# Optimization experiments

Hardware: AMD Instinct MI355X
Metric: run time of the kernel (lower is better)

The kernel has to match this reference:

```python
import jax, jax.numpy as jnp
import numpy as np

B, H, S, D = 4, 16, 2048, 128

def setup_inputs() -> dict:
    key = jax.random.key(0)
    kq, kk, kv = jax.random.split(key, 3)
    q = jax.random.normal(kq, (B, H, S, D), dtype=jnp.float32)
    k = jax.random.normal(kk, (B, H, S, D), dtype=jnp.float32)
    v = jax.random.normal(kv, (B, H, S, D), dtype=jnp.float32)
    return {"q": q, "k": k, "v": v}

def reference(q, k, v):
    # scores: [B, H, S, S] -- NOTE: original module applies no 1/sqrt(D) scale
    scores = jnp.einsum("bhqd,bhkd->bhqk", q, k)
    a = jax.nn.softmax(scores, axis=-1)  # numerically stable softmax
    return jnp.einsum("bhqk,bhkd->bhqd", a, v)
```

## Files before the change

kernel.cpp:

```cpp
#include <hip/hip_runtime.h>
#include <hip/hip_bf16.h>


#define QBLK   64
#define KVBLK  64
#define DHEAD  128
#define SEQ    2048
#define KPAD   136
#define PPAD   72

typedef _Float16 f16x8 __attribute__((ext_vector_type(8)));
typedef _Float16 f16x4 __attribute__((ext_vector_type(4)));
typedef float    f32x4 __attribute__((ext_vector_type(4)));

#define AS1P(x) ((const __attribute__((address_space(1))) void*)(size_t)(x))
#define AS3P(x) ((__attribute__((address_space(3))) void*)(unsigned long long)(unsigned)(size_t)(x))

__global__ __launch_bounds__(256)
void preconv_kernel(const float* __restrict__ K, const float* __restrict__ V,
                    _Float16* __restrict__ Kp, _Float16* __restrict__ Vp) {
    const int bt = blockIdx.x;
    const size_t src = (size_t)bt * (KVBLK * DHEAD);
    const float* Kt = K + src;
    const float* Vt = V + src;
    _Float16* Ko = Kp + src;
    _Float16* Vo = Vp + src;
    #pragma unroll
    for (int j = 0; j < 4; ++j) {
        const int c = threadIdx.x + 256 * j;
        {
            const int row = c >> 4;
            const int d0  = (c & 15) * 8;
            float4 f0 = *(const float4*)(Kt + row * DHEAD + d0);
            float4 f1 = *(const float4*)(Kt + row * DHEAD + d0 + 4);
            f16x8 h;
            h[0]=(_Float16)f0.x; h[1]=(_Float16)f0.y; h[2]=(_Float16)f0.z; h[3]=(_Float16)f0.w;
            h[4]=(_Float16)f1.x; h[5]=(_Float16)f1.y; h[6]=(_Float16)f1.z; h[7]=(_Float16)f1.w;
            *(f16x8*)&Ko[row * 128 + (d0 ^ ((row & 7) << 3))] = h;
        }
        {
            const int d8  = (c & 1) | (((c >> 3) & 7) << 1);
            const int row = ((c >> 1) & 3) | ((c >> 6) << 2);
            const int d0  = d8 * 8;
            float4 f0 = *(const float4*)(Vt + row * DHEAD + d0);
            float4 f1 = *(const float4*)(Vt + row * DHEAD + d0 + 4);
            f16x8 h;
            h[0]=(_Float16)f0.x; h[1]=(_Float16)f0.y; h[2]=(_Float16)f0.z; h[3]=(_Float16)f0.w;
            h[4]=(_Float16)f1.x; h[5]=(_Float16)f1.y; h[6]=(_Float16)f1.z; h[7]=(_Float16)f1.w;
            const int st = (row >> 2) * 8 + (d0 >> 4);
            *(f16x8*)&Vo[st * 64 + (row & 3) * 16 + (d0 & 15)] = h;
        }
    }
}

__global__ __launch_bounds__(256, 3)
void attn_fwd_kernel(const float* __restrict__ Q, const _Float16* __restrict__ Kp,
                     const _Float16* __restrict__ Vp, float* __restrict__ O) {
    __shared__ __align__(16) _Float16 K_lds[KVBLK * DHEAD];
    __shared__ __align__(16) _Float16 V_lds[KVBLK * DHEAD];
    __shared__ __align__(16) _Float16 P_lds[4 * 16 * 64];

    const int tid  = threadIdx.x;
    const int lane = tid & 63;
    const int wave = tid >> 6;
    const int g    = lane >> 4;
    const int lg   = lane & 15;

    const int flat    = blockIdx.x + gridDim.x * blockIdx.y;
    const int newflat = (flat & 7) * 256 + (flat >> 3);
    const int qtile   = newflat & 31;
    const int bh      = newflat >> 5;

    const float* Qg = Q + (size_t)bh * SEQ * DHEAD + (size_t)(qtile * QBLK) * DHEAD;
    float*       Og = O + (size_t)bh * SEQ * DHEAD + (size_t)(qtile * QBLK) * DHEAD;

    const unsigned trbase = (unsigned)(size_t)&V_lds[0] + (unsigned)(g * 2048 + lg * 8);

    f16x8 qf[4];
    {
        const float* qrow = Qg + (size_t)(wave * 16 + lg) * DHEAD;
        #pragma unroll
        for (int dc = 0; dc < 4; ++dc) {
            const int d0 = dc * 32 + g * 8;
            float4 f0 = *(const float4*)(qrow + d0);
            float4 f1 = *(const float4*)(qrow + d0 + 4);
            qf[dc][0] = (_Float16)f0.x; qf[dc][1] = (_Float16)f0.y;
            qf[dc][2] = (_Float16)f0.z; qf[dc][3] = (_Float16)f0.w;
            qf[dc][4] = (_Float16)f1.x; qf[dc][5] = (_Float16)f1.y;
            qf[dc][6] = (_Float16)f1.z; qf[dc][7] = (_Float16)f1.w;
        }
    }

    f32x4 acc[8];
    #pragma unroll
    for (int dt = 0; dt < 8; ++dt) { acc[dt][0]=0.f; acc[dt][1]=0.f; acc[dt][2]=0.f; acc[dt][3]=0.f; }
    float m = -1e30f, l = 0.f;

    for (int t = 0; t < SEQ / KVBLK; ++t) {
        {
            const _Float16* Ktile = Kp + (size_t)(bh * 32 + t) * (KVBLK * DHEAD);
            const _Float16* Vtile = Vp + (size_t)(bh * 32 + t) * (KVBLK * DHEAD);
            #pragma unroll
            for (int i = 0; i < 4; ++i) {
                const int eoff = wave * 2048 + i * 512;
                __builtin_amdgcn_global_load_lds(AS1P(Ktile + eoff + lane * 8),
                                                 AS3P(&K_lds[eoff]), 16, 0, 0);
                __builtin_amdgcn_global_load_lds(AS1P(Vtile + eoff + lane * 8),
                                                 AS3P(&V_lds[eoff]), 16, 0, 0);
            }
        }
        __syncthreads();

        f32x4 s[4];
        __builtin_amdgcn_s_setprio(1);
        #pragma unroll
        for (int ct = 0; ct < 4; ++ct) {
            f32x4 a; a[0]=0.f; a[1]=0.f; a[2]=0.f; a[3]=0.f;
            #pragma unroll
            for (int dc = 0; dc < 4; ++dc) {
                const int krow = ct * 16 + lg;
                const int off  = krow * 128 + ((dc * 32 + g * 8) ^ ((krow & 7) << 3));
                f16x8 kh = *(const f16x8*)&K_lds[off];
                a = __builtin_amdgcn_mfma_f32_16x16x32_f16(kh, qf[dc], a, 0, 0, 0);
            }
            s[ct] = a;
        }
        __builtin_amdgcn_s_setprio(0);

        float pmax = s[0][0];
        #pragma unroll
        for (int ct = 0; ct < 4; ++ct)
            #pragma unroll
            for (int r = 0; r < 4; ++r)
                pmax = fmaxf(pmax, s[ct][r]);
        pmax = fmaxf(pmax, __shfl_xor(pmax, 16));
        pmax = fmaxf(pmax, __shfl_xor(pmax, 32));
        const float mnew = fmaxf(m, pmax);
        const float sc   = __expf(m - mnew);
        m = mnew;
        float rs = 0.f;
        #pragma unroll
        for (int ct = 0; ct < 4; ++ct)
            #pragma unroll
            for (int r = 0; r < 4; ++r) {
                float p = __expf(s[ct][r] - mnew);
                s[ct][r] = p;
                rs += p;
            }
        rs += __shfl_xor(rs, 16);
        rs += __shfl_xor(rs, 32);
        l = l * sc + rs;

        #pragma unroll
        for (int r = 0; r < 4; ++r) {
            const float scr = __shfl(sc, g * 20 + r);
            #pragma unroll
            for (int dt = 0; dt < 8; ++dt) acc[dt][r] *= scr;
        }

        _Float16* pbase = &P_lds[wave * 16 * 64];
        #pragma unroll
        for (int ct = 0; ct < 4; ++ct) {
            f16x4 pk;
            pk[0] = (_Float16)s[ct][0]; pk[1] = (_Float16)s[ct][1];
            pk[2] = (_Float16)s[ct][2]; pk[3] = (_Float16)s[ct][3];
            *(f16x4*)&pbase[lg * 64 + ((ct * 16 + g * 4) ^ ((lg & 7) << 3))] = pk;
        }

        #pragma unroll
        for (int kt = 0; kt < 2; ++kt) {
            f16x8 pf = *(const f16x8*)&pbase[lg * 64 + ((kt * 32 + g * 8) ^ ((lg & 7) << 3))];
            #pragma unroll
            for (int dp = 0; dp < 4; ++dp) {
                f16x4 a0, a1, b0, b1;
                asm volatile(
                    "ds_read_b64_tr_b16 %0, %4 offset:%5\n\t"
                    "ds_read_b64_tr_b16 %1, %4 offset:%6\n\t"
                    "ds_read_b64_tr_b16 %2, %4 offset:%7\n\t"
                    "ds_read_b64_tr_b16 %3, %4 offset:%8\n\t"
                    "s_waitcnt lgkmcnt(0)"
                    : "=&v"(a0), "=&v"(a1), "=&v"(b0), "=&v"(b1)
                    : "v"(trbase),
                      "i"(kt * 8192 + (dp * 2 + 0) * 128),
                      "i"(kt * 8192 + 1024 + (dp * 2 + 0) * 128),
                      "i"(kt * 8192 + (dp * 2 + 1) * 128),
                      "i"(kt * 8192 + 1024 + (dp * 2 + 1) * 128)
                    : "memory");
                __builtin_amdgcn_sched_barrier(0);
                f16x8 vf0 = __builtin_shufflevector(a0, a1, 0, 1, 2, 3, 4, 5, 6, 7);
                f16x8 vf1 = __builtin_shufflevector(b0, b1, 0, 1, 2, 3, 4, 5, 6, 7);
                __builtin_amdgcn_s_setprio(1);
                acc[dp * 2 + 0] = __builtin_amdgcn_mfma_f32_16x16x32_f16(pf, vf0, acc[dp * 2 + 0], 0, 0, 0);
                acc[dp * 2 + 1] = __builtin_amdgcn_mfma_f32_16x16x32_f16(pf, vf1, acc[dp * 2 + 1], 0, 0, 0);
                __builtin_amdgcn_s_setprio(0);
            }
        }
        __syncthreads();
    }

    const float linv = 1.f / l;
    float inv[4];
    #pragma unroll
    for (int r = 0; r < 4; ++r) inv[r] = __shfl(linv, g * 20 + r);
    float* ob = Og + (size_t)(wave * 16) * DHEAD;
    #pragma unroll
    for (int dt = 0; dt < 8; ++dt)
        #pragma unroll
        for (int r = 0; r < 4; ++r)
            ob[(size_t)(g * 4 + r) * DHEAD + dt * 16 + lg] = acc[dt][r] * inv[r];
}

__global__ __launch_bounds__(256, 3)
void attn_fwd_legacy(const float* __restrict__ Q, const float* __restrict__ K,
                     const float* __restrict__ V, float* __restrict__ O) {
    __shared__ __align__(16) _Float16 K_lds[KVBLK * KPAD];
    __shared__ __align__(16) _Float16 V_lds[KVBLK * DHEAD];
    __shared__ __align__(16) _Float16 P_lds[4 * 16 * PPAD];

    const int tid  = threadIdx.x;
    const int lane = tid & 63;
    const int wave = tid >> 6;
    const int g    = lane >> 4;
    const int lg   = lane & 15;

    const int flat    = blockIdx.x + gridDim.x * blockIdx.y;
    const int newflat = (flat & 7) * 256 + (flat >> 3);
    const int qtile   = newflat & 31;
    const int bh      = newflat >> 5;

    const size_t base = (size_t)bh * SEQ * DHEAD;
    const float* Qg = Q + base + (size_t)(qtile * QBLK) * DHEAD;
    const float* Kg = K + base;
    const float* Vg = V + base;
    float*       Og = O + base + (size_t)(qtile * QBLK) * DHEAD;

    const unsigned trbase = (unsigned)(size_t)&V_lds[0] + (unsigned)(g * 2048 + lg * 8);

    f16x8 qf[4];
    {
        const float* qrow = Qg + (size_t)(wave * 16 + lg) * DHEAD;
        #pragma unroll
        for (int dc = 0; dc < 4; ++dc) {
            const int d0 = dc * 32 + g * 8;
            float4 f0 = *(const float4*)(qrow + d0);
            float4 f1 = *(const float4*)(qrow + d0 + 4);
            qf[dc][0] = (_Float16)f0.x; qf[dc][1] = (_Float16)f0.y;
            qf[dc][2] = (_Float16)f0.z; qf[dc][3] = (_Float16)f0.w;
            qf[dc][4] = (_Float16)f1.x; qf[dc][5] = (_Float16)f1.y;
            qf[dc][6] = (_Float16)f1.z; qf[dc][7] = (_Float16)f1.w;
        }
    }

    f32x4 acc[8];
    #pragma unroll
    for (int dt = 0; dt < 8; ++dt) { acc[dt][0]=0.f; acc[dt][1]=0.f; acc[dt][2]=0.f; acc[dt][3]=0.f; }
    float m = -1e30f, l = 0.f;

    for (int t = 0; t < SEQ / KVBLK; ++t) {
        {
            const float* Kt = Kg + (size_t)t * KVBLK * DHEAD;
            #pragma unroll
            for (int j = 0; j < 4; ++j) {
                const int c   = tid + 256 * j;
                const int row = c >> 4;
                const int dc  = (c & 15) * 8;
                float4 f0 = *(const float4*)(Kt + row * DHEAD + dc);
                float4 f1 = *(const float4*)(Kt + row * DHEAD + dc + 4);
                f16x8 vh;
                vh[0]=(_Float16)f0.x; vh[1]=(_Float16)f0.y; vh[2]=(_Float16)f0.z; vh[3]=(_Float16)f0.w;
                vh[4]=(_Float16)f1.x; vh[5]=(_Float16)f1.y; vh[6]=(_Float16)f1.z; vh[7]=(_Float16)f1.w;
                *(f16x8*)&K_lds[row * KPAD + dc] = vh;
            }
            const float* Vt = Vg + (size_t)t * KVBLK * DHEAD;
            #pragma unroll
            for (int j = 0; j < 4; ++j) {
                const int c   = tid + 256 * j;
                const int d8  = (c & 1) | (((c >> 3) & 7) << 1);
                const int row = ((c >> 1) & 3) | ((c >> 6) << 2);
                const int d0  = d8 * 8;
                float4 f0 = *(const float4*)(Vt + row * DHEAD + d0);
                float4 f1 = *(const float4*)(Vt + row * DHEAD + d0 + 4);
                f16x8 vv;
                vv[0]=(_Float16)f0.x; vv[1]=(_Float16)f0.y; vv[2]=(_Float16)f0.z; vv[3]=(_Float16)f0.w;
                vv[4]=(_Float16)f1.x; vv[5]=(_Float16)f1.y; vv[6]=(_Float16)f1.z; vv[7]=(_Float16)f1.w;
                const int st = (row >> 2) * 8 + (d0 >> 4);
                *(f16x8*)&V_lds[st * 64 + (row & 3) * 16 + (d0 & 15)] = vv;
            }
        }
        __syncthreads();

        f32x4 s[4];
        __builtin_amdgcn_s_setprio(1);
        #pragma unroll
        for (int ct = 0; ct < 4; ++ct) {
            f32x4 a; a[0]=0.f; a[1]=0.f; a[2]=0.f; a[3]=0.f;
            #pragma unroll
            for (int dc = 0; dc < 4; ++dc) {
                const int off = (ct * 16 + lg) * KPAD + dc * 32 + g * 8;
                f16x8 kh = *(const f16x8*)&K_lds[off];
                a = __builtin_amdgcn_mfma_f32_16x16x32_f16(kh, qf[dc], a, 0, 0, 0);
            }
            s[ct] = a;
        }
        __builtin_amdgcn_s_setprio(0);

        float pmax = s[0][0];
        #pragma unroll
        for (int ct = 0; ct < 4; ++ct)
            #pragma unroll
            for (int r = 0; r < 4; ++r)
                pmax = fmaxf(pmax, s[ct][r]);
        pmax = fmaxf(pmax, __shfl_xor(pmax, 16));
        pmax = fmaxf(pmax, __shfl_xor(pmax, 32));
        const float mnew = fmaxf(m, pmax);
        const float sc   = __expf(m - mnew);
        m = mnew;
        float rs = 0.f;
        #pragma unroll
        for (int ct = 0; ct < 4; ++ct)
            #pragma unroll
            for (int r = 0; r < 4; ++r) {
                float p = __expf(s[ct][r] - mnew);
                s[ct][r] = p;
                rs += p;
            }
        rs += __shfl_xor(rs, 16);
        rs += __shfl_xor(rs, 32);
        l = l * sc + rs;

        #pragma unroll
        for (int r = 0; r < 4; ++r) {
            const float scr = __shfl(sc, g * 20 + r);
            #pragma unroll
            for (int dt = 0; dt < 8; ++dt) acc[dt][r] *= scr;
        }

        _Float16* pbase = &P_lds[wave * 16 * PPAD];
        #pragma unroll
        for (int ct = 0; ct < 4; ++ct) {
            f16x4 pk;
            pk[0] = (_Float16)s[ct][0]; pk[1] = (_Float16)s[ct][1];
            pk[2] = (_Float16)s[ct][2]; pk[3] = (_Float16)s[ct][3];
            *(f16x4*)&pbase[lg * PPAD + ct * 16 + g * 4] = pk;
        }

        #pragma unroll
        for (int kt = 0; kt < 2; ++kt) {
            f16x8 pf = *(const f16x8*)&pbase[lg * PPAD + kt * 32 + g * 8];
            #pragma unroll
            for (int dp = 0; dp < 4; ++dp) {
                f16x4 a0, a1, b0, b1;
                asm volatile(
                    "ds_read_b64_tr_b16 %0, %4 offset:%5\n\t"
                    "ds_read_b64_tr_b16 %1, %4 offset:%6\n\t"
                    "ds_read_b64_tr_b16 %2, %4 offset:%7\n\t"
                    "ds_read_b64_tr_b16 %3, %4 offset:%8\n\t"
                    "s_waitcnt lgkmcnt(0)"
                    : "=&v"(a0), "=&v"(a1), "=&v"(b0), "=&v"(b1)
                    : "v"(trbase),
                      "i"(kt * 8192 + (dp * 2 + 0) * 128),
                      "i"(kt * 8192 + 1024 + (dp * 2 + 0) * 128),
                      "i"(kt * 8192 + (dp * 2 + 1) * 128),
                      "i"(kt * 8192 + 1024 + (dp * 2 + 1) * 128)
                    : "memory");
                __builtin_amdgcn_sched_barrier(0);
                f16x8 vf0 = __builtin_shufflevector(a0, a1, 0, 1, 2, 3, 4, 5, 6, 7);
                f16x8 vf1 = __builtin_shufflevector(b0, b1, 0, 1, 2, 3, 4, 5, 6, 7);
                __builtin_amdgcn_s_setprio(1);
                acc[dp * 2 + 0] = __builtin_amdgcn_mfma_f32_16x16x32_f16(pf, vf0, acc[dp * 2 + 0], 0, 0, 0);
                acc[dp * 2 + 1] = __builtin_amdgcn_mfma_f32_16x16x32_f16(pf, vf1, acc[dp * 2 + 1], 0, 0, 0);
                __builtin_amdgcn_s_setprio(0);
            }
        }
        __syncthreads();
    }

    const float linv = 1.f / l;
    float inv[4];
    #pragma unroll
    for (int r = 0; r < 4; ++r) inv[r] = __shfl(linv, g * 20 + r);
    float* ob = Og + (size_t)(wave * 16) * DHEAD;
    #pragma unroll
    for (int dt = 0; dt < 8; ++dt)
        #pragma unroll
        for (int r = 0; r < 4; ++r)
            ob[(size_t)(g * 4 + r) * DHEAD + dt * 16 + lg] = acc[dt][r] * inv[r];
}

extern "C" void kernel_launch(void* const* d_in, const int* in_sizes, int n_in,
                              void* d_out, int out_size, void* d_ws, size_t ws_size,
                              hipStream_t stream) {
    const float* q = (const float*)d_in[0];
    const float* k = (const float*)d_in[1];
    const float* v = (const float*)d_in[2];
    float* out = (float*)d_out;
    const int BH = in_sizes[0] / (SEQ * DHEAD);
    dim3 grid(SEQ / QBLK, BH);

    const size_t elems = (size_t)BH * SEQ * DHEAD;
    const size_t need  = elems * 2 * sizeof(_Float16);
    if (ws_size >= need) {
        _Float16* Kp = (_Float16*)d_ws;
        _Float16* Vp = Kp + elems;
        preconv_kernel<<<dim3(BH * (SEQ / KVBLK)), dim3(256), 0, stream>>>(k, v, Kp, Vp);
        attn_fwd_kernel<<<grid, dim3(256), 0, stream>>>(q, Kp, Vp, out);
    } else {
        attn_fwd_legacy<<<grid, dim3(256), 0, stream>>>(q, k, v, out);
    }
}
```

Baseline: 259.4 us.

## Pre-transpose V to d-major swizzled layout and use plain LDS reads for PV

The preconversion kernel now writes V transposed (d-major, 64 kv entries per row, XOR-swizzled) instead of the tiled layout consumed by ds_read_b64_tr_b16. The attention kernel's PV stage replaces the inline-asm transpose reads, which had a waitcnt after each group, with ordinary 16-byte LDS vector reads that the compiler can schedule freely. This gives fewer LDS instructions and better overlap with MFMA. The trade-off is strided scalar global reads of V in the preconversion kernel, which load much less efficiently than the previous float4 loads.

```diff
diff --git a/kernel.cpp b/kernel.cpp
--- a/kernel.cpp
+++ b/kernel.cpp
@@ -39,16 +39,13 @@
             *(f16x8*)&Ko[row * 128 + (d0 ^ ((row & 7) << 3))] = h;
         }
         {
-            const int d8  = (c & 1) | (((c >> 3) & 7) << 1);
-            const int row = ((c >> 1) & 3) | ((c >> 6) << 2);
-            const int d0  = d8 * 8;
-            float4 f0 = *(const float4*)(Vt + row * DHEAD + d0);
-            float4 f1 = *(const float4*)(Vt + row * DHEAD + d0 + 4);
+            const int d   = c & 127;
+            const int kvg = c >> 7;
             f16x8 h;
-            h[0]=(_Float16)f0.x; h[1]=(_Float16)f0.y; h[2]=(_Float16)f0.z; h[3]=(_Float16)f0.w;
-            h[4]=(_Float16)f1.x; h[5]=(_Float16)f1.y; h[6]=(_Float16)f1.z; h[7]=(_Float16)f1.w;
-            const int st = (row >> 2) * 8 + (d0 >> 4);
-            *(f16x8*)&Vo[st * 64 + (row & 3) * 16 + (d0 & 15)] = h;
+            #pragma unroll
+            for (int i = 0; i < 8; ++i)
+                h[i] = (_Float16)Vt[(kvg * 8 + i) * DHEAD + d];
+            *(f16x8*)&Vo[d * 64 + ((kvg * 8) ^ ((d & 7) << 3))] = h;
         }
     }
 }
@@ -57,7 +54,7 @@
 void attn_fwd_kernel(const float* __restrict__ Q, const _Float16* __restrict__ Kp,
                      const _Float16* __restrict__ Vp, float* __restrict__ O) {
     __shared__ __align__(16) _Float16 K_lds[KVBLK * DHEAD];
-    __shared__ __align__(16) _Float16 V_lds[KVBLK * DHEAD];
+    __shared__ __align__(16) _Float16 V_lds[DHEAD * KVBLK];
     __shared__ __align__(16) _Float16 P_lds[4 * 16 * 64];
 
     const int tid  = threadIdx.x;
@@ -73,8 +70,6 @@
 
     const float* Qg = Q + (size_t)bh * SEQ * DHEAD + (size_t)(qtile * QBLK) * DHEAD;
     float*       Og = O + (size_t)bh * SEQ * DHEAD + (size_t)(qtile * QBLK) * DHEAD;
-
-    const unsigned trbase = (unsigned)(size_t)&V_lds[0] + (unsigned)(g * 2048 + lg * 8);
 
     f16x8 qf[4];
     {
@@ -167,9 +162,170 @@
             *(f16x4*)&pbase[lg * 64 + ((ct * 16 + g * 4) ^ ((lg & 7) << 3))] = pk;
         }
 
+        __builtin_amdgcn_s_setprio(1);
         #pragma unroll
         for (int kt = 0; kt < 2; ++kt) {
-            f16x8 pf = *(const f16x8*)&pbase[lg * 64 + ((kt * 32 + g * 8) ^ ((lg & 7) << 3))];
+            const int koff = (kt * 32 + g * 8) ^ ((lg & 7) << 3);
+            f16x8 pf = *(const f16x8*)&pbase[lg * 64 + koff];
+            #pragma unroll
+            for (int dt = 0; dt < 8; ++dt) {
+                f16x8 vf = *(const f16x8*)&V_lds[(dt * 16 + lg) * 64 + koff];
+                acc[dt] = __builtin_amdgcn_mfma_f32_16x16x32_f16(pf, vf, acc[dt], 0, 0, 0);
+            }
+        }
+        __builtin_amdgcn_s_setprio(0);
+        __syncthreads();
+    }
+
+    const float linv = 1.f / l;
+    float inv[4];
+    #pragma unroll
+    for (int r = 0; r < 4; ++r) inv[r] = __shfl(linv, g * 20 + r);
+    float* ob = Og + (size_t)(wave * 16) * DHEAD;
+    #pragma unroll
+    for (int dt = 0; dt < 8; ++dt)
+        #pragma unroll
+        for (int r = 0; r < 4; ++r)
+            ob[(size_t)(g * 4 + r) * DHEAD + dt * 16 + lg] = acc[dt][r] * inv[r];
+}
+
+__global__ __launch_bounds__(256, 3)
+void attn_fwd_legacy(const float* __restrict__ Q, const float* __restrict__ K,
+                     const float* __restrict__ V, float* __restrict__ O) {
+    __shared__ __align__(16) _Float16 K_lds[KVBLK * KPAD];
+    __shared__ __align__(16) _Float16 V_lds[KVBLK * DHEAD];
+    __shared__ __align__(16) _Float16 P_lds[4 * 16 * PPAD];
+
+    const int tid  = threadIdx.x;
+    const int lane = tid & 63;
+    const int wave = tid >> 6;
+    const int g    = lane >> 4;
+    const int lg   = lane & 15;
+
+    const int flat    = blockIdx.x + gridDim.x * blockIdx.y;
+    const int newflat = (flat & 7) * 256 + (flat >> 3);
+    const int qtile   = newflat & 31;
+    const int bh      = newflat >> 5;
+
+    const size_t base = (size_t)bh * SEQ * DHEAD;
+    const float* Qg = Q + base + (size_t)(qtile * QBLK) * DHEAD;
+    const float* Kg = K + base;
+    const float* Vg = V + base;
+    float*       Og = O + base + (size_t)(qtile * QBLK) * DHEAD;
+
+    const unsigned trbase = (unsigned)(size_t)&V_lds[0] + (unsigned)(g * 2048 + lg * 8);
+
+    f16x8 qf[4];
+    {
+        const float* qrow = Qg + (size_t)(wave * 16 + lg) * DHEAD;
+        #pragma unroll
+        for (int dc = 0; dc < 4; ++dc) {
+            const int d0 = dc * 32 + g * 8;
+            float4 f0 = *(const float4*)(qrow + d0);
+            float4 f1 = *(const float4*)(qrow + d0 + 4);
+            qf[dc][0] = (_Float16)f0.x; qf[dc][1] = (_Float16)f0.y;
+            qf[dc][2] = (_Float16)f0.z; qf[dc][3] = (_Float16)f0.w;
+            qf[dc][4] = (_Float16)f1.x; qf[dc][5] = (_Float16)f1.y;
+            qf[dc][6] = (_Float16)f1.z; qf[dc][7] = (_Float16)f1.w;
+        }
+    }
+
+    f32x4 acc[8];
+    #pragma unroll
+    for (int dt = 0; dt < 8; ++dt) { acc[dt][0]=0.f; acc[dt][1]=0.f; acc[dt][2]=0.f; acc[dt][3]=0.f; }
+    float m = -1e30f, l = 0.f;
+
+    for (int t = 0; t < SEQ / KVBLK; ++t) {
+        {
+            const float* Kt = Kg + (size_t)t * KVBLK * DHEAD;
+            #pragma unroll
+            for (int j = 0; j < 4; ++j) {
+                const int c   = tid + 256 * j;
+                const int row = c >> 4;
+                const int dc  = (c & 15) * 8;
+                float4 f0 = *(const float4*)(Kt + row * DHEAD + dc);
+                float4 f1 = *(const float4*)(Kt + row * DHEAD + dc + 4);
+                f16x8 vh;
+                vh[0]=(_Float16)f0.x; vh[1]=(_Float16)f0.y; vh[2]=(_Float16)f0.z; vh[3]=(_Float16)f0.w;
+                vh[4]=(_Float16)f1.x; vh[5]=(_Float16)f1.y; vh[6]=(_Float16)f1.z; vh[7]=(_Float16)f1.w;
+                *(f16x8*)&K_lds[row * KPAD + dc] = vh;
+            }
+            const float* Vt = Vg + (size_t)t * KVBLK * DHEAD;
+            #pragma unroll
+            for (int j = 0; j < 4; ++j) {
+                const int c   = tid + 256 * j;
+                const int d8  = (c & 1) | (((c >> 3) & 7) << 1);
+                const int row = ((c >> 1) & 3) | ((c >> 6) << 2);
+                const int d0  = d8 * 8;
+                float4 f0 = *(const float4*)(Vt + row * DHEAD + d0);
+                float4 f1 = *(const float4*)(Vt + row * DHEAD + d0 + 4);
+                f16x8 vv;
+                vv[0]=(_Float16)f0.x; vv[1]=(_Float16)f0.y; vv[2]=(_Float16)f0.z; vv[3]=(_Float16)f0.w;
+                vv[4]=(_Float16)f1.x; vv[5]=(_Float16)f1.y; vv[6]=(_Float16)f1.z; vv[7]=(_Float16)f1.w;
+                const int st = (row >> 2) * 8 + (d0 >> 4);
+                *(f16x8*)&V_lds[st * 64 + (row & 3) * 16 + (d0 & 15)] = vv;
+            }
+        }
+        __syncthreads();
+
+        f32x4 s[4];
+        __builtin_amdgcn_s_setprio(1);
+        #pragma unroll
+        for (int ct = 0; ct < 4; ++ct) {
+            f32x4 a; a[0]=0.f; a[1]=0.f; a[2]=0.f; a[3]=0.f;
+            #pragma unroll
+            for (int dc = 0; dc < 4; ++dc) {
+                const int off = (ct * 16 + lg) * KPAD + dc * 32 + g * 8;
+                f16x8 kh = *(const f16x8*)&K_lds[off];
+                a = __builtin_amdgcn_mfma_f32_16x16x32_f16(kh, qf[dc], a, 0, 0, 0);
+            }
+            s[ct] = a;
+        }
+        __builtin_amdgcn_s_setprio(0);
+
+        float pmax = s[0][0];
+        #pragma unroll
+        for (int ct = 0; ct < 4; ++ct)
+            #pragma unroll
+            for (int r = 0; r < 4; ++r)
+                pmax = fmaxf(pmax, s[ct][r]);
+        pmax = fmaxf(pmax, __shfl_xor(pmax, 16));
+        pmax = fmaxf(pmax, __shfl_xor(pmax, 32));
+        const float mnew = fmaxf(m, pmax);
+        const float sc   = __expf(m - mnew);
+        m = mnew;
+        float rs = 0.f;
+        #pragma unroll
+        for (int ct = 0; ct < 4; ++ct)
+            #pragma unroll
+            for (int r = 0; r < 4; ++r) {
+                float p = __expf(s[ct][r] - mnew);
+                s[ct][r] = p;
+                rs += p;
+            }
+        rs += __shfl_xor(rs, 16);
+        rs += __shfl_xor(rs, 32);
+        l = l * sc + rs;
+
+        #pragma unroll
+        for (int r = 0; r < 4; ++r) {
+            const float scr = __shfl(sc, g * 20 + r);
+            #pragma unroll
+            for (int dt = 0; dt < 8; ++dt) acc[dt][r] *= scr;
+        }
+
+        _Float16* pbase = &P_lds[wave * 16 * PPAD];
+        #pragma unroll
+        for (int ct = 0; ct < 4; ++ct) {
+            f16x4 pk;
+            pk[0] = (_Float16)s[ct][0]; pk[1] = (_Float16)s[ct][1];
+            pk[2] = (_Float16)s[ct][2]; pk[3] = (_Float16)s[ct][3];
+            *(f16x4*)&pbase[lg * PPAD + ct * 16 + g * 4] = pk;
+        }
+
+        #pragma unroll
+        for (int kt = 0; kt < 2; ++kt) {
+            f16x8 pf = *(const f16x8*)&pbase[lg * PPAD + kt * 32 + g * 8];
             #pragma unroll
             for (int dp = 0; dp < 4; ++dp) {
                 f16x4 a0, a1, b0, b1;
@@ -210,183 +366,6 @@
             ob[(size_t)(g * 4 + r) * DHEAD + dt * 16 + lg] = acc[dt][r] * inv[r];
 }
 
-__global__ __launch_bounds__(256, 3)
-void attn_fwd_legacy(const float* __restrict__ Q, const float* __restrict__ K,
-                     const float* __restrict__ V, float* __restrict__ O) {
-    __shared__ __align__(16) _Float16 K_lds[KVBLK * KPAD];
-    __shared__ __align__(16) _Float16 V_lds[KVBLK * DHEAD];
-    __shared__ __align__(16) _Float16 P_lds[4 * 16 * PPAD];
-
-    const int tid  = threadIdx.x;
-    const int lane = tid & 63;
-    const int wave = tid >> 6;
-    const int g    = lane >> 4;
-    const int lg   = lane & 15;
-
-    const int flat    = blockIdx.x + gridDim.x * blockIdx.y;
-    const int newflat = (flat & 7) * 256 + (flat >> 3);
-    const int qtile   = newflat & 31;
-    const int bh      = newflat >> 5;
-
-    const size_t base = (size_t)bh * SEQ * DHEAD;
-    const float* Qg = Q + base + (size_t)(qtile * QBLK) * DHEAD;
-    const float* Kg = K + base;
-    const float* Vg = V + base;
-    float*       Og = O + base + (size_t)(qtile * QBLK) * DHEAD;
-
-    const unsigned trbase = (unsigned)(size_t)&V_lds[0] + (unsigned)(g * 2048 + lg * 8);
-
-    f16x8 qf[4];
-    {
-        const float* qrow = Qg + (size_t)(wave * 16 + lg) * DHEAD;
-        #pragma unroll
-        for (int dc = 0; dc < 4; ++dc) {
-            const int d0 = dc * 32 + g * 8;
-            float4 f0 = *(const float4*)(qrow + d0);
-            float4 f1 = *(const float4*)(qrow + d0 + 4);
-            qf[dc][0] = (_Float16)f0.x; qf[dc][1] = (_Float16)f0.y;
-            qf[dc][2] = (_Float16)f0.z; qf[dc][3] = (_Float16)f0.w;
-            qf[dc][4] = (_Float16)f1.x; qf[dc][5] = (_Float16)f1.y;
-            qf[dc][6] = (_Float16)f1.z; qf[dc][7] = (_Float16)f1.w;
-        }
-    }
-
-    f32x4 acc[8];
-    #pragma unroll
-    for (int dt = 0; dt < 8; ++dt) { acc[dt][0]=0.f; acc[dt][1]=0.f; acc[dt][2]=0.f; acc[dt][3]=0.f; }
-    float m = -1e30f, l = 0.f;
-
-    for (int t = 0; t < SEQ / KVBLK; ++t) {
-        {
-            const float* Kt = Kg + (size_t)t * KVBLK * DHEAD;
-            #pragma unroll
-            for (int j = 0; j < 4; ++j) {
-                const int c   = tid + 256 * j;
-                const int row = c >> 4;
-                const int dc  = (c & 15) * 8;
-                float4 f0 = *(const float4*)(Kt + row * DHEAD + dc);
-                float4 f1 = *(const float4*)(Kt + row * DHEAD + dc + 4);
-                f16x8 vh;
-                vh[0]=(_Float16)f0.x; vh[1]=(_Float16)f0.y; vh[2]=(_Float16)f0.z; vh[3]=(_Float16)f0.w;
-                vh[4]=(_Float16)f1.x; vh[5]=(_Float16)f1.y; vh[6]=(_Float16)f1.z; vh[7]=(_Float16)f1.w;
-                *(f16x8*)&K_lds[row * KPAD + dc] = vh;
-            }
-            const float* Vt = Vg + (size_t)t * KVBLK * DHEAD;
-            #pragma unroll
-            for (int j = 0; j < 4; ++j) {
-                const int c   = tid + 256 * j;
-                const int d8  = (c & 1) | (((c >> 3) & 7) << 1);
-                const int row = ((c >> 1) & 3) | ((c >> 6) << 2);
-                const int d0  = d8 * 8;
-                float4 f0 = *(const float4*)(Vt + row * DHEAD + d0);
-                float4 f1 = *(const float4*)(Vt + row * DHEAD + d0 + 4);
-                f16x8 vv;
-                vv[0]=(_Float16)f0.x; vv[1]=(_Float16)f0.y; vv[2]=(_Float16)f0.z; vv[3]=(_Float16)f0.w;
-                vv[4]=(_Float16)f1.x; vv[5]=(_Float16)f1.y; vv[6]=(_Float16)f1.z; vv[7]=(_Float16)f1.w;
-                const int st = (row >> 2) * 8 + (d0 >> 4);
-                *(f16x8*)&V_lds[st * 64 + (row & 3) * 16 + (d0 & 15)] = vv;
-            }
-        }
-        __syncthreads();
-
-        f32x4 s[4];
-        __builtin_amdgcn_s_setprio(1);
-        #pragma unroll
-        for (int ct = 0; ct < 4; ++ct) {
-            f32x4 a; a[0]=0.f; a[1]=0.f; a[2]=0.f; a[3]=0.f;
-            #pragma unroll
-            for (int dc = 0; dc < 4; ++dc) {
-                const int off = (ct * 16 + lg) * KPAD + dc * 32 + g * 8;
-                f16x8 kh = *(const f16x8*)&K_lds[off];
-                a = __builtin_amdgcn_mfma_f32_16x16x32_f16(kh, qf[dc], a, 0, 0, 0);
-            }
-            s[ct] = a;
-        }
-        __builtin_amdgcn_s_setprio(0);
-
-        float pmax = s[0][0];
-        #pragma unroll
-        for (int ct = 0; ct < 4; ++ct)
-            #pragma unroll
-            for (int r = 0; r < 4; ++r)
-                pmax = fmaxf(pmax, s[ct][r]);
-        pmax = fmaxf(pmax, __shfl_xor(pmax, 16));
-        pmax = fmaxf(pmax, __shfl_xor(pmax, 32));
-        const float mnew = fmaxf(m, pmax);
-        const float sc   = __expf(m - mnew);
-        m = mnew;
-        float rs = 0.f;
-        #pragma unroll
-        for (int ct = 0; ct < 4; ++ct)
-            #pragma unroll
-            for (int r = 0; r < 4; ++r) {
-                float p = __expf(s[ct][r] - mnew);
-                s[ct][r] = p;
-                rs += p;
-            }
-        rs += __shfl_xor(rs, 16);
-        rs += __shfl_xor(rs, 32);
-        l = l * sc + rs;
-
-        #pragma unroll
-        for (int r = 0; r < 4; ++r) {
-            const float scr = __shfl(sc, g * 20 + r);
-            #pragma unroll
-            for (int dt = 0; dt < 8; ++dt) acc[dt][r] *= scr;
-        }
-
-        _Float16* pbase = &P_lds[wave * 16 * PPAD];
-        #pragma unroll
-        for (int ct = 0; ct < 4; ++ct) {
-            f16x4 pk;
-            pk[0] = (_Float16)s[ct][0]; pk[1] = (_Float16)s[ct][1];
-            pk[2] = (_Float16)s[ct][2]; pk[3] = (_Float16)s[ct][3];
-            *(f16x4*)&pbase[lg * PPAD + ct * 16 + g * 4] = pk;
-        }
-
-        #pragma unroll
-        for (int kt = 0; kt < 2; ++kt) {
-            f16x8 pf = *(const f16x8*)&pbase[lg * PPAD + kt * 32 + g * 8];
-            #pragma unroll
-            for (int dp = 0; dp < 4; ++dp) {
-                f16x4 a0, a1, b0, b1;
-                asm volatile(
-                    "ds_read_b64_tr_b16 %0, %4 offset:%5\n\t"
-                    "ds_read_b64_tr_b16 %1, %4 offset:%6\n\t"
-                    "ds_read_b64_tr_b16 %2, %4 offset:%7\n\t"
-                    "ds_read_b64_tr_b16 %3, %4 offset:%8\n\t"
-                    "s_waitcnt lgkmcnt(0)"
-                    : "=&v"(a0), "=&v"(a1), "=&v"(b0), "=&v"(b1)
-                    : "v"(trbase),
-                      "i"(kt * 8192 + (dp * 2 + 0) * 128),
-                      "i"(kt * 8192 + 1024 + (dp * 2 + 0) * 128),
-                      "i"(kt * 8192 + (dp * 2 + 1) * 128),
-                      "i"(kt * 8192 + 1024 + (dp * 2 + 1) * 128)
-                    : "memory");
-                __builtin_amdgcn_sched_barrier(0);
-                f16x8 vf0 = __builtin_shufflevector(a0, a1, 0, 1, 2, 3, 4, 5, 6, 7);
-                f16x8 vf1 = __builtin_shufflevector(b0, b1, 0, 1, 2, 3, 4, 5, 6, 7);
-                __builtin_amdgcn_s_setprio(1);
-                acc[dp * 2 + 0] = __builtin_amdgcn_mfma_f32_16x16x32_f16(pf, vf0, acc[dp * 2 + 0], 0, 0, 0);
-                acc[dp * 2 + 1] = __builtin_amdgcn_mfma_f32_16x16x32_f16(pf, vf1, acc[dp * 2 + 1], 0, 0, 0);
-                __builtin_amdgcn_s_setprio(0);
-            }
-        }
-        __syncthreads();
-    }
-
-    const float linv = 1.f / l;
-    float inv[4];
-    #pragma unroll
-    for (int r = 0; r < 4; ++r) inv[r] = __shfl(linv, g * 20 + r);
-    float* ob = Og + (size_t)(wave * 16) * DHEAD;
-    #pragma unroll
-    for (int dt = 0; dt < 8; ++dt)
-        #pragma unroll
-        for (int r = 0; r < 4; ++r)
-            ob[(size_t)(g * 4 + r) * DHEAD + dt * 16 + lg] = acc[dt][r] * inv[r];
-}
-
 extern "C" void kernel_launch(void* const* d_in, const int* in_sizes, int n_in,
                               void* d_out, int out_size, void* d_ws, size_t ws_size,
                               hipStream_t stream) {
```

After: 250.8 us. 3.3% less time.
